# Performance work log

Measured on AMD Instinct MI355X. Metric: run time of the kernel, lower is better.

The kernel has to match this reference:

```python
import jax, jax.numpy as jnp
import numpy as np
from jax import lax

START_TAG = 29
STOP_TAG = 30
PAD_TAG = 31
NEG_INF = -10000.0


def setup_inputs() -> dict:
    key = jax.random.key(0)
    k_feat, k_trans, k_len = jax.random.split(key, 3)
    S, B, T = 1024, 1024, 32
    feats = jax.random.normal(k_feat, (S, B, T), dtype=jnp.float32)
    # left-aligned padding mask with random lengths in [S//2, S]
    lengths = jax.random.randint(k_len, (B,), S // 2, S + 1)
    mask = (jnp.arange(S)[:, None] < lengths[None, :]).astype(jnp.float32)  # [S,B]
    transitions = jax.random.normal(k_trans, (T, T), dtype=jnp.float32)
    # replicate the constraint initialization from __init__
    transitions = transitions.at[START_TAG, :].set(NEG_INF)
    transitions = transitions.at[:, STOP_TAG].set(NEG_INF)
    transitions = transitions.at[:, PAD_TAG].set(NEG_INF)
    transitions = transitions.at[PAD_TAG, :].set(NEG_INF)
    transitions = transitions.at[PAD_TAG, STOP_TAG].set(0.0)
    transitions = transitions.at[PAD_TAG, PAD_TAG].set(0.0)
    # zero emissions at padded steps, as _get_lstm_features does (feats * mask)
    feats = feats * mask[:, :, None]
    return {"feats": feats, "mask": mask, "transitions": transitions}


def reference(feats, mask, transitions):
    """CRF forward algorithm (log partition) + Viterbi max-score scan.

    feats: [S, B, T] emission scores, mask: [S, B] float, transitions: [T, T]
    (transitions[i, j] = score of transitioning from tag j to tag i).
    Returns (logZ [B], best_score [B], pointers [S, B, T] int32).
    """
    S, B, T = feats.shape

    alpha0 = jnp.full((B, T), NEG_INF, dtype=feats.dtype).at[:, START_TAG].set(0.0)

    def fwd_step(alpha, xs):
        feat, m = xs  # feat [B,T], m [B]
        # alpha_t[b, i, j] = alpha[b, j] + transitions[i, j] + feat[b, i]
        alpha_t = alpha[:, None, :] + transitions[None, :, :] + feat[:, :, None]
        new = jax.nn.logsumexp(alpha_t, axis=-1)  # [B,T]
        m = m[:, None]
        return new * m + alpha * (1.0 - m), None

    alpha, _ = lax.scan(fwd_step, alpha0, (feats, mask))
    logZ = jax.nn.logsumexp(alpha + transitions[STOP_TAG][None, :], axis=-1)  # [B]

    def vit_step(scores, xs):
        feat, m = xs
        scores_t = scores[:, None, :] + transitions[None, :, :]  # [B,T,T]
        best = jnp.max(scores_t, axis=-1)                        # [B,T]
        ptr = jnp.argmax(scores_t, axis=-1).astype(jnp.int32)    # [B,T]
        scores_t = best + feat
        m = m[:, None]
        return scores_t * m + scores * (1.0 - m), ptr

    scores0 = jnp.full((B, T), NEG_INF, dtype=feats.dtype).at[:, START_TAG].set(0.0)
    scores, pointers = lax.scan(vit_step, scores0, (feats, mask))
    scores = scores + transitions[STOP_TAG][None, :]
    best_score = jnp.max(scores, axis=-1)  # [B]
    return logZ, best_score, pointers
```

## Files before the change

kernel.cpp:

```cpp
#include <hip/hip_runtime.h>


#define SS 1024
#define BB 1024
#define TT 32
#define POFF (2 * BB)

__global__ __launch_bounds__(64) void crf2_kernel(
    const float* __restrict__ feats,
    const float* __restrict__ mask,
    const float* __restrict__ trans,
    float* __restrict__ out) {

  const int l  = threadIdx.x;
  const int h  = l >> 5;
  const int i  = l & 31;
  const int b0 = blockIdx.x * 2;
  const int b  = b0 + h;

  __shared__ __align__(16) float row[64];

  const float* fbase = feats + (size_t)b0 * TT + l;
  const float* mbase = mask + b;
  const float t_stop = trans[30 * TT + i];

  float f0[4], m0[4], f1[4], m1[4];
#pragma unroll
  for (int u = 0; u < 4; ++u) {
    f0[u] = fbase[(size_t)u * BB * TT];
    m0[u] = mbase[(size_t)u * BB];
    f1[u] = fbase[(size_t)(u + 4) * BB * TT];
    m1[u] = mbase[(size_t)(u + 4) * BB];
  }

  if (blockIdx.y == 0) {
    float er[32];
#pragma unroll
    for (int k = 0; k < 32; ++k)
      er[k] = __expf(trans[i * TT + k]);

    float alpha = (i == 29) ? 0.0f : -10000.0f;
    float M = 0.0f;

#pragma unroll 1
    for (int s = 0; s < SS; s += 4) {
      float nf[4], nm[4];
#pragma unroll
      for (int u = 0; u < 4; ++u) {
        int su = (s + 8 + u < SS) ? (s + 8 + u) : 0;
        nf[u] = fbase[(size_t)su * BB * TT];
        nm[u] = mbase[(size_t)su * BB];
      }
#pragma unroll
      for (int u = 0; u < 4; ++u) {
        bool act = (m0[u] != 0.0f);
        if (__ballot(act) == 0ull) goto fwd_done;
        float p = __expf(alpha - M);
        row[l] = p;
        __builtin_amdgcn_wave_barrier();
        const float4* q = (const float4*)&row[h * 32];
        float4 q0 = q[0], q1 = q[1], q2 = q[2], q3 = q[3];
        float4 q4 = q[4], q5 = q[5], q6 = q[6], q7 = q[7];
        __builtin_amdgcn_wave_barrier();
        float a0 = er[0] * q0.x, a1 = er[1] * q0.y;
        float a2 = er[2] * q0.z, a3 = er[3] * q0.w;
        a0 = fmaf(er[4],  q1.x, a0); a1 = fmaf(er[5],  q1.y, a1);
        a2 = fmaf(er[6],  q1.z, a2); a3 = fmaf(er[7],  q1.w, a3);
        a0 = fmaf(er[8],  q2.x, a0); a1 = fmaf(er[9],  q2.y, a1);
        a2 = fmaf(er[10], q2.z, a2); a3 = fmaf(er[11], q2.w, a3);
        a0 = fmaf(er[12], q3.x, a0); a1 = fmaf(er[13], q3.y, a1);
        a2 = fmaf(er[14], q3.z, a2); a3 = fmaf(er[15], q3.w, a3);
        a0 = fmaf(er[16], q4.x, a0); a1 = fmaf(er[17], q4.y, a1);
        a2 = fmaf(er[18], q4.z, a2); a3 = fmaf(er[19], q4.w, a3);
        a0 = fmaf(er[20], q5.x, a0); a1 = fmaf(er[21], q5.y, a1);
        a2 = fmaf(er[22], q5.z, a2); a3 = fmaf(er[23], q5.w, a3);
        a0 = fmaf(er[24], q6.x, a0); a1 = fmaf(er[25], q6.y, a1);
        a2 = fmaf(er[26], q6.z, a2); a3 = fmaf(er[27], q6.w, a3);
        a0 = fmaf(er[28], q7.x, a0); a1 = fmaf(er[29], q7.y, a1);
        a2 = fmaf(er[30], q7.z, a2); a3 = fmaf(er[31], q7.w, a3);
        float D = (a0 + a1) + (a2 + a3);
        float nv = M + f0[u] + __logf(D);
        alpha = act ? nv : alpha;
        M = M + fmaxf(__logf(q0.x), -20.0f);
      }
#pragma unroll
      for (int u = 0; u < 4; ++u) {
        f0[u] = f1[u]; m0[u] = m1[u]; f1[u] = nf[u]; m1[u] = nm[u];
      }
    }
fwd_done:
    {
      float v = alpha + t_stop;
      float M2 = v;
#pragma unroll
      for (int d = 1; d < 32; d <<= 1) M2 = fmaxf(M2, __shfl_xor(M2, d, 64));
      float e = __expf(v - M2);
#pragma unroll
      for (int d = 1; d < 32; d <<= 1) e += __shfl_xor(e, d, 64);
      if (i == 0) out[b] = M2 + __logf(e);
    }
    return;
  }

  {
    float tr[32];
#pragma unroll
    for (int k = 0; k < 32; ++k) tr[k] = trans[i * TT + k];

    float sc = (i == 29) ? 0.0f : -10000.0f;
    int s_exit = SS;

    auto vstep = [&](float& best, int& ptr) {
      row[l] = sc;
      __builtin_amdgcn_wave_barrier();
      const float4* q = (const float4*)&row[h * 32];
      float4 q0 = q[0], q1 = q[1], q2 = q[2], q3 = q[3];
      float4 q4 = q[4], q5 = q[5], q6 = q[6], q7 = q[7];
      __builtin_amdgcn_wave_barrier();
      float v[32];
      v[0]  = q0.x + tr[0];  v[1]  = q0.y + tr[1];
      v[2]  = q0.z + tr[2];  v[3]  = q0.w + tr[3];
      v[4]  = q1.x + tr[4];  v[5]  = q1.y + tr[5];
      v[6]  = q1.z + tr[6];  v[7]  = q1.w + tr[7];
      v[8]  = q2.x + tr[8];  v[9]  = q2.y + tr[9];
      v[10] = q2.z + tr[10]; v[11] = q2.w + tr[11];
      v[12] = q3.x + tr[12]; v[13] = q3.y + tr[13];
      v[14] = q3.z + tr[14]; v[15] = q3.w + tr[15];
      v[16] = q4.x + tr[16]; v[17] = q4.y + tr[17];
      v[18] = q4.z + tr[18]; v[19] = q4.w + tr[19];
      v[20] = q5.x + tr[20]; v[21] = q5.y + tr[21];
      v[22] = q5.z + tr[22]; v[23] = q5.w + tr[23];
      v[24] = q6.x + tr[24]; v[25] = q6.y + tr[25];
      v[26] = q6.z + tr[26]; v[27] = q6.w + tr[27];
      v[28] = q7.x + tr[28]; v[29] = q7.y + tr[29];
      v[30] = q7.z + tr[30]; v[31] = q7.w + tr[31];
      int ix[32];
#pragma unroll
      for (int k = 0; k < 32; ++k) ix[k] = k;
#pragma unroll
      for (int st = 1; st < 32; st <<= 1) {
#pragma unroll
        for (int k = 0; k < 32; k += 2 * st) {
          bool t = v[k + st] > v[k];
          v[k]  = t ? v[k + st] : v[k];
          ix[k] = t ? ix[k + st] : ix[k];
        }
      }
      best = v[0];
      ptr  = ix[0];
    };

#pragma unroll 1
    for (int s = 0; s < SS; s += 4) {
      float nf[4], nm[4];
#pragma unroll
      for (int u = 0; u < 4; ++u) {
        int su = (s + 8 + u < SS) ? (s + 8 + u) : 0;
        nf[u] = fbase[(size_t)su * BB * TT];
        nm[u] = mbase[(size_t)su * BB];
      }
#pragma unroll
      for (int u = 0; u < 4; ++u) {
        bool act = (m0[u] != 0.0f);
        if (__ballot(act) == 0ull) { s_exit = s + u; goto vit_tail; }
        float best; int ptr;
        vstep(best, ptr);
        out[POFF + (size_t)(s + u) * BB * TT + b0 * TT + l] = (float)ptr;
        sc = act ? best + f0[u] : sc;
      }
#pragma unroll
      for (int u = 0; u < 4; ++u) {
        f0[u] = f1[u]; m0[u] = m1[u]; f1[u] = nf[u]; m1[u] = nm[u];
      }
    }
vit_tail:
    {
      float tb; int tp;
      vstep(tb, tp);
      float tj = (float)tp;
      for (int s2 = s_exit; s2 < SS; ++s2)
        out[POFF + (size_t)s2 * BB * TT + b0 * TT + l] = tj;

      float w = sc + t_stop;
#pragma unroll
      for (int d = 1; d < 32; d <<= 1) w = fmaxf(w, __shfl_xor(w, d, 64));
      if (i == 0) out[BB + b] = w;
    }
  }
}

extern "C" void kernel_launch(void* const* d_in, const int* in_sizes, int n_in,
                              void* d_out, int out_size, void* d_ws, size_t ws_size,
                              hipStream_t stream) {
  const float* feats = (const float*)d_in[0];
  const float* msk   = (const float*)d_in[1];
  const float* trans = (const float*)d_in[2];
  float* out = (float*)d_out;
  (void)in_sizes; (void)n_in; (void)out_size; (void)d_ws; (void)ws_size;
  crf2_kernel<<<dim3(BB / 2, 2), dim3(64), 0, stream>>>(feats, msk, trans, out);
}
```

Before: 577.2 us.

## Carry forward recursion in linear probability space with deferred log scaling

The forward logsumexp recursion now keeps normalised probabilities p and a running log scale C instead of log-space alpha. This removes the per-step exp(alpha-M) and log(D) from the serial dependency chain, replacing them with a reciprocal and multiplies, and moves the log off the critical path. The prefetch loop is restructured into two ping-pong register buffers with early-exit checks only at each 4-step group start. Launch bounds also request one block per SIMD. Risks are numeric underflow or overflow in linear space, bounded only by the clamp on q0.x.

After: 545.8 us. 5.4% less time.

```diff
diff --git a/kernel.cpp b/kernel.cpp
--- a/kernel.cpp
+++ b/kernel.cpp
@@ -6,7 +6,15 @@
 #define TT 32
 #define POFF (2 * BB)
 
-__global__ __launch_bounds__(64) void crf2_kernel(
+static __device__ __forceinline__ float fastrcp(float x) {
+#if __has_builtin(__builtin_amdgcn_rcpf)
+  return __builtin_amdgcn_rcpf(x);
+#else
+  return 1.0f / x;
+#endif
+}
+
+__global__ __launch_bounds__(64, 1) void crf3_kernel(
     const float* __restrict__ feats,
     const float* __restrict__ mask,
     const float* __restrict__ trans,
@@ -24,13 +32,13 @@
   const float* mbase = mask + b;
   const float t_stop = trans[30 * TT + i];
 
-  float f0[4], m0[4], f1[4], m1[4];
+  float fA[4], mA[4], fB[4], mB[4];
 #pragma unroll
   for (int u = 0; u < 4; ++u) {
-    f0[u] = fbase[(size_t)u * BB * TT];
-    m0[u] = mbase[(size_t)u * BB];
-    f1[u] = fbase[(size_t)(u + 4) * BB * TT];
-    m1[u] = mbase[(size_t)(u + 4) * BB];
+    fA[u] = fbase[(size_t)u * (BB * TT)];
+    mA[u] = mbase[(size_t)u * BB];
+    fB[u] = fbase[(size_t)(u + 4) * (BB * TT)];
+    mB[u] = mbase[(size_t)(u + 4) * BB];
   }
 
   if (blockIdx.y == 0) {
@@ -39,57 +47,66 @@
     for (int k = 0; k < 32; ++k)
       er[k] = __expf(trans[i * TT + k]);
 
-    float alpha = (i == 29) ? 0.0f : -10000.0f;
-    float M = 0.0f;
+    float p = (i == 29) ? 1.0f : 0.0f;
+    float C = 0.0f;
+
+    auto fstep = [&](float fv, float mv) {
+      bool act = (mv != 0.0f);
+      float ef = __expf(fv);
+      row[l] = p;
+      __builtin_amdgcn_wave_barrier();
+      const float4* q = (const float4*)&row[h * 32];
+      float4 q0 = q[0], q1 = q[1], q2 = q[2], q3 = q[3];
+      float4 q4 = q[4], q5 = q[5], q6 = q[6], q7 = q[7];
+      __builtin_amdgcn_wave_barrier();
+      float q0c = fmaxf(q0.x, 1e-20f);
+      float r = fastrcp(q0c);
+      float a0 = er[0] * q0.x, a1 = er[1] * q0.y;
+      float a2 = er[2] * q0.z, a3 = er[3] * q0.w;
+      a0 = fmaf(er[4],  q1.x, a0); a1 = fmaf(er[5],  q1.y, a1);
+      a2 = fmaf(er[6],  q1.z, a2); a3 = fmaf(er[7],  q1.w, a3);
+      a0 = fmaf(er[8],  q2.x, a0); a1 = fmaf(er[9],  q2.y, a1);
+      a2 = fmaf(er[10], q2.z, a2); a3 = fmaf(er[11], q2.w, a3);
+      a0 = fmaf(er[12], q3.x, a0); a1 = fmaf(er[13], q3.y, a1);
+      a2 = fmaf(er[14], q3.z, a2); a3 = fmaf(er[15], q3.w, a3);
+      a0 = fmaf(er[16], q4.x, a0); a1 = fmaf(er[17], q4.y, a1);
+      a2 = fmaf(er[18], q4.z, a2); a3 = fmaf(er[19], q4.w, a3);
+      a0 = fmaf(er[20], q5.x, a0); a1 = fmaf(er[21], q5.y, a1);
+      a2 = fmaf(er[22], q5.z, a2); a3 = fmaf(er[23], q5.w, a3);
+      a0 = fmaf(er[24], q6.x, a0); a1 = fmaf(er[25], q6.y, a1);
+      a2 = fmaf(er[26], q6.z, a2); a3 = fmaf(er[27], q6.w, a3);
+      a0 = fmaf(er[28], q7.x, a0); a1 = fmaf(er[29], q7.y, a1);
+      a2 = fmaf(er[30], q7.z, a2); a3 = fmaf(er[31], q7.w, a3);
+      float D = (a0 + a1) + (a2 + a3);
+      float pn = D * r * ef;
+      p = act ? pn : p;
+      C += act ? __logf(q0c) : 0.0f;
+    };
 
 #pragma unroll 1
-    for (int s = 0; s < SS; s += 4) {
-      float nf[4], nm[4];
-#pragma unroll
-      for (int u = 0; u < 4; ++u) {
-        int su = (s + 8 + u < SS) ? (s + 8 + u) : 0;
-        nf[u] = fbase[(size_t)su * BB * TT];
-        nm[u] = mbase[(size_t)su * BB];
-      }
-#pragma unroll
-      for (int u = 0; u < 4; ++u) {
-        bool act = (m0[u] != 0.0f);
-        if (__ballot(act) == 0ull) goto fwd_done;
-        float p = __expf(alpha - M);
-        row[l] = p;
-        __builtin_amdgcn_wave_barrier();
-        const float4* q = (const float4*)&row[h * 32];
-        float4 q0 = q[0], q1 = q[1], q2 = q[2], q3 = q[3];
-        float4 q4 = q[4], q5 = q[5], q6 = q[6], q7 = q[7];
-        __builtin_amdgcn_wave_barrier();
-        float a0 = er[0] * q0.x, a1 = er[1] * q0.y;
-        float a2 = er[2] * q0.z, a3 = er[3] * q0.w;
-        a0 = fmaf(er[4],  q1.x, a0); a1 = fmaf(er[5],  q1.y, a1);
-        a2 = fmaf(er[6],  q1.z, a2); a3 = fmaf(er[7],  q1.w, a3);
-        a0 = fmaf(er[8],  q2.x, a0); a1 = fmaf(er[9],  q2.y, a1);
-        a2 = fmaf(er[10], q2.z, a2); a3 = fmaf(er[11], q2.w, a3);
-        a0 = fmaf(er[12], q3.x, a0); a1 = fmaf(er[13], q3.y, a1);
-        a2 = fmaf(er[14], q3.z, a2); a3 = fmaf(er[15], q3.w, a3);
-        a0 = fmaf(er[16], q4.x, a0); a1 = fmaf(er[17], q4.y, a1);
-        a2 = fmaf(er[18], q4.z, a2); a3 = fmaf(er[19], q4.w, a3);
-        a0 = fmaf(er[20], q5.x, a0); a1 = fmaf(er[21], q5.y, a1);
-        a2 = fmaf(er[22], q5.z, a2); a3 = fmaf(er[23], q5.w, a3);
-        a0 = fmaf(er[24], q6.x, a0); a1 = fmaf(er[25], q6.y, a1);
-        a2 = fmaf(er[26], q6.z, a2); a3 = fmaf(er[27], q6.w, a3);
-        a0 = fmaf(er[28], q7.x, a0); a1 = fmaf(er[29], q7.y, a1);
-        a2 = fmaf(er[30], q7.z, a2); a3 = fmaf(er[31], q7.w, a3);
-        float D = (a0 + a1) + (a2 + a3);
-        float nv = M + f0[u] + __logf(D);
-        alpha = act ? nv : alpha;
-        M = M + fmaxf(__logf(q0.x), -20.0f);
-      }
-#pragma unroll
-      for (int u = 0; u < 4; ++u) {
-        f0[u] = f1[u]; m0[u] = m1[u]; f1[u] = nf[u]; m1[u] = nm[u];
+    for (int s = 0; s < SS; s += 8) {
+      if (__ballot(mA[0] != 0.0f) == 0ull) goto fwd_done;
+#pragma unroll
+      for (int u = 0; u < 4; ++u) fstep(fA[u], mA[u]);
+#pragma unroll
+      for (int u = 0; u < 4; ++u) {
+        int su = s + 8 + u; su = (su < SS) ? su : 0;
+        fA[u] = fbase[(size_t)su * (BB * TT)];
+        mA[u] = mbase[(size_t)su * BB];
+      }
+      if (__ballot(mB[0] != 0.0f) == 0ull) goto fwd_done;
+#pragma unroll
+      for (int u = 0; u < 4; ++u) fstep(fB[u], mB[u]);
+#pragma unroll
+      for (int u = 0; u < 4; ++u) {
+        int su = s + 12 + u; su = (su < SS) ? su : 0;
+        fB[u] = fbase[(size_t)su * (BB * TT)];
+        mB[u] = mbase[(size_t)su * BB];
       }
     }
 fwd_done:
     {
+      float alpha = C + __logf(p);
       float v = alpha + t_stop;
       float M2 = v;
 #pragma unroll
@@ -151,35 +168,43 @@
     };
 
 #pragma unroll 1
-    for (int s = 0; s < SS; s += 4) {
-      float nf[4], nm[4];
-#pragma unroll
-      for (int u = 0; u < 4; ++u) {
-        int su = (s + 8 + u < SS) ? (s + 8 + u) : 0;
-        nf[u] = fbase[(size_t)su * BB * TT];
-        nm[u] = mbase[(size_t)su * BB];
-      }
-#pragma unroll
-      for (int u = 0; u < 4; ++u) {
-        bool act = (m0[u] != 0.0f);
-        if (__ballot(act) == 0ull) { s_exit = s + u; goto vit_tail; }
+    for (int s = 0; s < SS; s += 8) {
+      if (__ballot(mA[0] != 0.0f) == 0ull) { s_exit = s; goto vtail; }
+#pragma unroll
+      for (int u = 0; u < 4; ++u) {
         float best; int ptr;
         vstep(best, ptr);
-        out[POFF + (size_t)(s + u) * BB * TT + b0 * TT + l] = (float)ptr;
-        sc = act ? best + f0[u] : sc;
-      }
-#pragma unroll
-      for (int u = 0; u < 4; ++u) {
-        f0[u] = f1[u]; m0[u] = m1[u]; f1[u] = nf[u]; m1[u] = nm[u];
-      }
-    }
-vit_tail:
+        out[POFF + (size_t)(s + u) * (BB * TT) + b0 * TT + l] = (float)ptr;
+        sc = (mA[u] != 0.0f) ? (best + fA[u]) : sc;
+      }
+#pragma unroll
+      for (int u = 0; u < 4; ++u) {
+        int su = s + 8 + u; su = (su < SS) ? su : 0;
+        fA[u] = fbase[(size_t)su * (BB * TT)];
+        mA[u] = mbase[(size_t)su * BB];
+      }
+      if (__ballot(mB[0] != 0.0f) == 0ull) { s_exit = s + 4; goto vtail; }
+#pragma unroll
+      for (int u = 0; u < 4; ++u) {
+        float best; int ptr;
+        vstep(best, ptr);
+        out[POFF + (size_t)(s + 4 + u) * (BB * TT) + b0 * TT + l] = (float)ptr;
+        sc = (mB[u] != 0.0f) ? (best + fB[u]) : sc;
+      }
+#pragma unroll
+      for (int u = 0; u < 4; ++u) {
+        int su = s + 12 + u; su = (su < SS) ? su : 0;
+        fB[u] = fbase[(size_t)su * (BB * TT)];
+        mB[u] = mbase[(size_t)su * BB];
+      }
+    }
+vtail:
     {
       float tb; int tp;
       vstep(tb, tp);
       float tj = (float)tp;
       for (int s2 = s_exit; s2 < SS; ++s2)
-        out[POFF + (size_t)s2 * BB * TT + b0 * TT + l] = tj;
+        out[POFF + (size_t)s2 * (BB * TT) + b0 * TT + l] = tj;
 
       float w = sc + t_stop;
 #pragma unroll
@@ -197,5 +222,5 @@
   const float* trans = (const float*)d_in[2];
   float* out = (float*)d_out;
   (void)in_sizes; (void)n_in; (void)out_size; (void)d_ws; (void)ws_size;
-  crf2_kernel<<<dim3(BB / 2, 2), dim3(64), 0, stream>>>(feats, msk, trans, out);
+  crf3_kernel<<<dim3(BB / 2, 2), dim3(64), 0, stream>>>(feats, msk, trans, out);
 }
```
